# Kernel tuning notes

Measured on AMD Instinct MI355X. Metric: run time of the kernel, lower is better.

Reference implementation:

```python
import jax, jax.numpy as jnp
import numpy as np

A = 128       # atom_fea_len
NBR = 41      # nbr_fea_len
H = 128       # h_fea_len_dist == h_fea_len_const
NCONV = 3
EPS = 1e-5    # BatchNorm eps


def leaky(x):
    return jnp.where(x >= 0, x, 0.01 * x)  # LeakyReLU(0.01)


def bn(x2d, g, b):
    # training-mode BatchNorm1d: batch statistics over dim 0 (biased variance)
    mu = x2d.mean(0)
    var = x2d.var(0)
    return g * (x2d - mu) * jax.lax.rsqrt(var + EPS) + b


def setup_inputs() -> dict:
    N, M = 20000, 12
    key = jax.random.key(0)
    ks = jax.random.split(key, 24)
    s = 0.02
    in2 = 2 * A + NBR  # 297
    d = {}
    d["atom_fea"] = jax.random.normal(ks[0], (N, 92), jnp.float32)
    d["nbr_fea"] = jax.random.uniform(ks[1], (N, M, NBR), dtype=jnp.float32)
    d["nbr_fea_offset"] = jax.random.normal(ks[2], (N, M, 3), jnp.float32)
    d["atom_pos"] = jax.random.normal(ks[3], (N, 3), jnp.float32) * 3.0
    d["cells"] = jnp.eye(3, dtype=jnp.float32) * 10.0 + 0.1 * jax.random.normal(ks[4], (3, 3), jnp.float32)
    d["nbr_fea_idx"] = jax.random.randint(ks[5], (N, M), 0, N)
    # embedding
    d["emb_W"] = s * jax.random.normal(ks[6], (A, 92), jnp.float32)
    d["emb_b"] = jnp.zeros((A,), jnp.float32)
    # conv layers (stacked)
    d["convs_W"] = s * jax.random.normal(ks[7], (NCONV, 2 * A, in2), jnp.float32)
    d["convs_b"] = jnp.zeros((NCONV, 2 * A), jnp.float32)
    d["convs_bn1_g"] = jnp.ones((NCONV, 2 * A), jnp.float32)
    d["convs_bn1_b"] = jnp.zeros((NCONV, 2 * A), jnp.float32)
    d["convs_bn2_g"] = jnp.ones((NCONV, A), jnp.float32)
    d["convs_bn2_b"] = jnp.zeros((NCONV, A), jnp.float32)
    # bond_distance head
    d["dist_W"] = s * jax.random.normal(ks[8], (H, in2), jnp.float32)
    d["dist_b"] = jnp.zeros((H,), jnp.float32)
    d["dist_bn_g"] = jnp.ones((H,), jnp.float32)
    d["dist_bn_b"] = jnp.zeros((H,), jnp.float32)
    d["dist2_W"] = s * jax.random.normal(ks[9], (1, H), jnp.float32)
    d["dist2_b"] = jnp.zeros((1,), jnp.float32)
    # bond_constant head
    d["const_W"] = s * jax.random.normal(ks[10], (H, in2), jnp.float32)
    d["const_b"] = jnp.zeros((H,), jnp.float32)
    d["const_bn_g"] = jnp.ones((H,), jnp.float32)
    d["const_bn_b"] = jnp.zeros((H,), jnp.float32)
    d["const2_W"] = s * jax.random.normal(ks[11], (1, H), jnp.float32)
    d["const2_b"] = jnp.zeros((1,), jnp.float32)
    return d


def _forward(atom_fea, nbr_fea, nbr_fea_offset, atom_pos, cells,
             emb_W, emb_b, convs_W, convs_b, convs_bn1_g, convs_bn1_b,
             convs_bn2_g, convs_bn2_b, dist_W, dist_b, dist_bn_g, dist_bn_b,
             dist2_W, dist2_b, const_W, const_b, const_bn_g, const_bn_b,
             const2_W, const2_b, nbr_fea_idx):
    N, M = nbr_fea_idx.shape
    af = atom_fea @ emb_W.T + emb_b  # (N, A) embedding

    # get_distance: PBC distance using fractional offsets and the cell matrix
    nbr_abs = atom_pos[nbr_fea_idx] + jnp.einsum('nmk,kd->nmd', nbr_fea_offset, cells)
    dvec = nbr_abs - atom_pos[:, None, :]
    distance = jnp.sqrt(jnp.sum(dvec * dvec, -1, keepdims=True) + 1e-12)  # (N, M, 1)

    # conv layers: gather -> concat -> linear -> bn -> gate -> sum -> bn -> residual
    for i in range(NCONV):
        total = jnp.concatenate([
            jnp.broadcast_to(af[:, None, :], (N, M, A)),
            af[nbr_fea_idx],
            nbr_fea], axis=2)                                   # (N, M, 2A+NBR)
        g = jnp.einsum('nmf,of->nmo', total, convs_W[i]) + convs_b[i]  # (N, M, 2A)
        g = bn(g.reshape(-1, 2 * A), convs_bn1_g[i], convs_bn1_b[i]).reshape(N, M, 2 * A)
        nbr_filter = jax.nn.sigmoid(g[..., :A])
        nbr_core = leaky(g[..., A:])
        summed = bn((nbr_filter * nbr_core).sum(1), convs_bn2_g[i], convs_bn2_b[i])
        af = leaky(af + summed)

    # bond features
    bond_fea = jnp.concatenate([
        jnp.broadcast_to(af[:, None, :], (N, M, A)),
        af[nbr_fea_idx],
        nbr_fea], axis=2)  # (N, M, 2A+NBR)

    # bond_distance head (LeakyReLU activations)
    bd = jnp.einsum('nmf,hf->nmh', bond_fea, dist_W) + dist_b
    bd = leaky(bn(bd.reshape(-1, H), dist_bn_g, dist_bn_b).reshape(N, M, H))
    bd = leaky(jnp.einsum('nmh,oh->nmo', bd, dist2_W) + dist2_b + distance)  # (N, M, 1)

    # bond_constant head (Softplus activations)
    bc = jnp.einsum('nmf,hf->nmh', bond_fea, const_W) + const_b
    bc = jax.nn.softplus(bn(bc.reshape(-1, H), const_bn_g, const_bn_b).reshape(N, M, H))
    bc = jax.nn.softplus(jnp.einsum('nmh,oh->nmo', bc, const2_W) + const2_b)  # (N, M, 1)

    return jnp.concatenate([bd, bc], axis=-1)  # (N, M, 2)


def reference(atom_fea, nbr_fea, nbr_fea_offset, atom_pos, cells,
              emb_W, emb_b, convs_W, convs_b, convs_bn1_g, convs_bn1_b,
              convs_bn2_g, convs_bn2_b, dist_W, dist_b, dist_bn_g, dist_bn_b,
              dist2_W, dist2_b, const_W, const_b, const_bn_g, const_bn_b,
              const2_W, const2_b, nbr_fea_idx):
    return _forward(atom_fea, nbr_fea, nbr_fea_offset, atom_pos, cells,
                    emb_W, emb_b, convs_W, convs_b, convs_bn1_g, convs_bn1_b,
                    convs_bn2_g, convs_bn2_b, dist_W, dist_b, dist_bn_g, dist_bn_b,
                    dist2_W, dist2_b, const_W, const_b, const_bn_g, const_bn_b,
                    const2_W, const2_b, nbr_fea_idx)
```

## Files before the change

kernel.cpp:

```cpp
#include <hip/hip_runtime.h>
#include <hip/hip_bf16.h>
#include <math.h>

typedef __hip_bfloat16 bf16;

#define AFEA 128
#define NBRF 41
#define IN2 297
#define KP 320
#define TSTR 328
#define ROWS 64
#define P1 64
#define P2 16

typedef __attribute__((ext_vector_type(8))) short bf16x8;
typedef __attribute__((ext_vector_type(4))) float f32x4;

__device__ __forceinline__ unsigned short bfbits(float x) {
    bf16 h = __float2bfloat16(x);
    return *(unsigned short*)&h;
}
__device__ __forceinline__ unsigned int pack2(float x, float y) {
    return (unsigned int)bfbits(x) | ((unsigned int)bfbits(y) << 16);
}
__device__ __forceinline__ float blo(unsigned int u) { return __uint_as_float(u << 16); }
__device__ __forceinline__ float bhi(unsigned int u) { return __uint_as_float(u & 0xffff0000u); }
__device__ __forceinline__ float leakyf(float x) { return x >= 0.f ? x : 0.01f * x; }
__device__ __forceinline__ float sigmoid_fast(float x) { return 1.f / (1.f + __expf(-x)); }
__device__ __forceinline__ float softplus_fast(float x) {
    return fmaxf(x, 0.f) + __logf(1.f + __expf(-fabsf(x)));
}

__global__ void nbr16_kernel(const float* __restrict__ nbr, unsigned short* __restrict__ nbr16,
                             int NM)
{
    int i = blockIdx.x * blockDim.x + threadIdx.x;
    if (i >= NM * 64) return;
    int k = i & 63, e = i >> 6;
    nbr16[i] = (k < NBRF) ? bfbits(nbr[(size_t)e * NBRF + k]) : 0;
}

__global__ __launch_bounds__(256) void embed_kernel(
    const float* __restrict__ xf, const float* __restrict__ W,
    const float* __restrict__ b, float* __restrict__ af,
    unsigned short* __restrict__ af16, int N)
{
    __shared__ float W_s[92 * 128];
    __shared__ float xs[16 * 92];
    int t = threadIdx.x;
    int n0 = blockIdx.x * 16;
    for (int i = t; i < 92 * 128; i += 256) {
        int o = i / 92, k = i - o * 92;
        W_s[k * 128 + o] = W[i];
    }
    for (int i = t; i < 16 * 92; i += 256) {
        int a = i / 92, k = i - a * 92;
        int n = n0 + a;
        xs[i] = (n < N) ? xf[(size_t)n * 92 + k] : 0.f;
    }
    __syncthreads();
    int o = t & 127, h = t >> 7;
    float bias = b[o];
    for (int a = h; a < 16; a += 2) {
        int n = n0 + a;
        if (n >= N) break;
        float acc = bias;
        const float* xr = xs + a * 92;
        #pragma unroll 4
        for (int k = 0; k < 92; k++) acc += xr[k] * W_s[k * 128 + o];
        af[(size_t)n * AFEA + o] = acc;
        af16[(size_t)n * AFEA + o] = bfbits(acc);
    }
}

__global__ void prep_kernel(const float* __restrict__ Wa, size_t offA,
                            const float* __restrict__ Wsrc, size_t offB,
                            unsigned short* __restrict__ Wb,
                            float* __restrict__ zbuf, int nz)
{
    int i = blockIdx.x * blockDim.x + threadIdx.x;
    if (i < nz) zbuf[i] = 0.f;
    if (i >= KP * 256) return;
    int t32 = i & 31;
    int c = (i >> 5) & 255;
    int kc = i >> 13;
    int k = kc * 32 + t32;
    float v = 0.f;
    if (k < IN2) v = (c < 128) ? Wa[offA + (size_t)c * IN2 + k]
                               : Wsrc[offB + (size_t)(c - 128) * IN2 + k];
    Wb[i] = bfbits(v);
}

__global__ __launch_bounds__(256, 3) void gemm_mfma_kernel(
    const unsigned short* __restrict__ af16, const unsigned short* __restrict__ nbr16,
    const int* __restrict__ idx, const unsigned short* __restrict__ Wb,
    const float* __restrict__ bias_a, size_t boffA,
    const float* __restrict__ bias_b, size_t boffB,
    unsigned short* __restrict__ g_t, float* __restrict__ part1,
    int NM, int M)
{
    __shared__ unsigned short a_tile[ROWS * TSTR];
    const int t = threadIdx.x;
    const int e0 = blockIdx.x * ROWS;

    const int l = t & 63, w = t >> 6;
    const int m16 = l & 15, q = l >> 4;
    const int colbase = w * 64;
    const unsigned short* bbase = Wb + (size_t)(colbase + m16) * 32 + q * 8;

    {
        int row = t >> 2, p = t & 3;
        int e = e0 + row;
        int n = e / M;
        int j = idx[e];
        const uint4* srcn = (const uint4*)(af16 + (size_t)n * AFEA);
        const uint4* srcj = (const uint4*)(af16 + (size_t)j * AFEA);
        const uint4* srcb = (const uint4*)(nbr16 + (size_t)e * 64);
        uint4* dst = (uint4*)(a_tile + row * TSTR);
        #pragma unroll
        for (int u = 0; u < 4; u++) dst[p + 4 * u] = srcn[p + 4 * u];
        #pragma unroll
        for (int u = 0; u < 4; u++) dst[16 + p + 4 * u] = srcj[p + 4 * u];
        #pragma unroll
        for (int u = 0; u < 2; u++) dst[32 + p + 4 * u] = srcb[p + 4 * u];
    }

    bf16x8 bcur[4], bnxt[4];
    #pragma unroll
    for (int ct = 0; ct < 4; ct++)
        bcur[ct] = *(const bf16x8*)(bbase + ct * 512);
    #pragma unroll
    for (int ct = 0; ct < 4; ct++)
        bnxt[ct] = *(const bf16x8*)(bbase + 8192 + ct * 512);

    __syncthreads();

    f32x4 acc[4][4];
    #pragma unroll
    for (int rt = 0; rt < 4; rt++)
        #pragma unroll
        for (int ct = 0; ct < 4; ct++) acc[rt][ct] = (f32x4)0.f;

    const unsigned short* abase = a_tile + m16 * TSTR + q * 8;

    #pragma unroll
    for (int kc = 0; kc < KP / 32; kc++) {
        bf16x8 a[4], b2[4];
        if (kc < KP / 32 - 2) {
            #pragma unroll
            for (int ct = 0; ct < 4; ct++)
                b2[ct] = *(const bf16x8*)(bbase + (kc + 2) * 8192 + ct * 512);
        }
        #pragma unroll
        for (int rt = 0; rt < 4; rt++)
            a[rt] = *(const bf16x8*)(abase + rt * 16 * TSTR + kc * 32);
        #pragma unroll
        for (int rt = 0; rt < 4; rt++)
            #pragma unroll
            for (int ct = 0; ct < 4; ct++)
                acc[rt][ct] = __builtin_amdgcn_mfma_f32_16x16x32_bf16(
                    a[rt], bcur[ct], acc[rt][ct], 0, 0, 0);
        if (kc < KP / 32 - 1) {
            #pragma unroll
            for (int ct = 0; ct < 4; ct++) bcur[ct] = bnxt[ct];
        }
        if (kc < KP / 32 - 2) {
            #pragma unroll
            for (int ct = 0; ct < 4; ct++) bnxt[ct] = b2[ct];
        }
    }

    float* pp = part1 + (size_t)(blockIdx.x & (P1 - 1)) * 512;
    #pragma unroll
    for (int ct = 0; ct < 4; ct++) {
        int col = colbase + ct * 16 + m16;
        float bias = (col < 128) ? bias_a[boffA + col] : bias_b[boffB + col - 128];
        float ps = 0.f, pq = 0.f;
        #pragma unroll
        for (int rt = 0; rt < 4; rt++) {
            float v0 = acc[rt][ct][0] + bias;
            float v1 = acc[rt][ct][1] + bias;
            float v2 = acc[rt][ct][2] + bias;
            float v3 = acc[rt][ct][3] + bias;
            ps += (v0 + v1) + (v2 + v3);
            pq += (v0 * v0 + v1 * v1) + (v2 * v2 + v3 * v3);
            uint2 pk;
            pk.x = pack2(v0, v1);
            pk.y = pack2(v2, v3);
            *(uint2*)(g_t + (size_t)col * NM + e0 + rt * 16 + q * 4) = pk;
        }
        ps += __shfl_xor(ps, 16); ps += __shfl_xor(ps, 32);
        pq += __shfl_xor(pq, 16); pq += __shfl_xor(pq, 32);
        if (q == 0) {
            atomicAdd(&pp[col], ps);
            atomicAdd(&pp[256 + col], pq);
        }
    }
}

__global__ __launch_bounds__(256) void gate_kernel(
    const unsigned short* __restrict__ gt, const float* __restrict__ part1,
    const float* __restrict__ gamma, const float* __restrict__ beta,
    float* __restrict__ summed, float* __restrict__ part2,
    float cnt1, int N, int M, int NM)
{
    __shared__ float affA[4 * 16], affC[4 * 16];
    int t = threadIdx.x, w = t >> 6, l = t & 63;
    int cp0 = (blockIdx.x & 3) * 16 + w * 4;
    int fch0 = 2 * cp0;

    if (l < 16) {
        int ch = (l < 8) ? (fch0 + l) : (128 + fch0 + (l - 8));
        float s = 0.f, qq = 0.f;
        #pragma unroll 8
        for (int p = 0; p < P1; p++) {
            s += part1[(size_t)p * 512 + ch];
            qq += part1[(size_t)p * 512 + 256 + ch];
        }
        float mean = s / cnt1;
        float var = fmaxf(qq / cnt1 - mean * mean, 0.f);
        float a = gamma[ch] * rsqrtf(var + 1e-5f);
        affA[w * 16 + l] = a;
        affC[w * 16 + l] = beta[ch] - mean * a;
    }
    __syncthreads();

    int n = (blockIdx.x >> 2) * 64 + l;
    bool act = (n < N);
    size_t col0 = (size_t)n * M;
    float* pp = part2 + (size_t)(blockIdx.x & (P2 - 1)) * 256;
    #pragma unroll
    for (int cpi = 0; cpi < 4; cpi++) {
        int chf = fch0 + 2 * cpi;
        int chc = 128 + chf;
        float s0 = 0.f, s1 = 0.f;
        if (act) {
            const uint2* rf0 = (const uint2*)(gt + (size_t)chf * NM + col0);
            const uint2* rf1 = (const uint2*)(gt + (size_t)(chf + 1) * NM + col0);
            const uint2* rc0 = (const uint2*)(gt + (size_t)chc * NM + col0);
            const uint2* rc1 = (const uint2*)(gt + (size_t)(chc + 1) * NM + col0);
            float aF0 = affA[w * 16 + 2 * cpi],     cF0 = affC[w * 16 + 2 * cpi];
            float aF1 = affA[w * 16 + 2 * cpi + 1], cF1 = affC[w * 16 + 2 * cpi + 1];
            float aC0 = affA[w * 16 + 8 + 2 * cpi],     cC0 = affC[w * 16 + 8 + 2 * cpi];
            float aC1 = affA[w * 16 + 8 + 2 * cpi + 1], cC1 = affC[w * 16 + 8 + 2 * cpi + 1];
            #pragma unroll
            for (int u = 0; u < 3; u++) {
                uint2 f0 = rf0[u], f1 = rf1[u], k0 = rc0[u], k1 = rc1[u];
                #pragma unroll
                for (int h = 0; h < 4; h++) {
                    unsigned int fw0 = (h < 2) ? f0.x : f0.y;
                    unsigned int fw1 = (h < 2) ? f1.x : f1.y;
                    unsigned int kw0 = (h < 2) ? k0.x : k0.y;
                    unsigned int kw1 = (h < 2) ? k1.x : k1.y;
                    float gf0 = (h & 1) ? bhi(fw0) : blo(fw0);
                    float gf1 = (h & 1) ? bhi(fw1) : blo(fw1);
                    float gc0 = (h & 1) ? bhi(kw0) : blo(kw0);
                    float gc1 = (h & 1) ? bhi(kw1) : blo(kw1);
                    s0 += sigmoid_fast(fmaf(aF0, gf0, cF0)) * leakyf(fmaf(aC0, gc0, cC0));
                    s1 += sigmoid_fast(fmaf(aF1, gf1, cF1)) * leakyf(fmaf(aC1, gc1, cC1));
                }
            }
            *(float2*)(summed + (size_t)n * AFEA + chf) = make_float2(s0, s1);
        }
        float q0 = s0 * s0, q1 = s1 * s1;
        #pragma unroll
        for (int sft = 32; sft > 0; sft >>= 1) {
            s0 += __shfl_xor(s0, sft);
            s1 += __shfl_xor(s1, sft);
            q0 += __shfl_xor(q0, sft);
            q1 += __shfl_xor(q1, sft);
        }
        if (l == 0) {
            atomicAdd(&pp[chf], s0);
            atomicAdd(&pp[chf + 1], s1);
            atomicAdd(&pp[128 + chf], q0);
            atomicAdd(&pp[128 + chf + 1], q1);
        }
    }
}

__global__ __launch_bounds__(256) void afup_kernel(
    float* __restrict__ af, unsigned short* __restrict__ af16,
    const float* __restrict__ summed, const float* __restrict__ part2,
    const float* __restrict__ gamma2, const float* __restrict__ beta2,
    float cnt2, int total)
{
    __shared__ float a2s[128], c2s[128];
    int t = threadIdx.x;
    if (t < 128) {
        float s = 0.f, qq = 0.f;
        #pragma unroll
        for (int p = 0; p < P2; p++) {
            s += part2[(size_t)p * 256 + t];
            qq += part2[(size_t)p * 256 + 128 + t];
        }
        float mean = s / cnt2;
        float var = fmaxf(qq / cnt2 - mean * mean, 0.f);
        float a = gamma2[t] * rsqrtf(var + 1e-5f);
        a2s[t] = a;
        c2s[t] = beta2[t] - mean * a;
    }
    __syncthreads();
    int o = t & 127;
    float a2 = a2s[o], c2 = c2s[o];
    int base = blockIdx.x * 2048 + t;
    #pragma unroll
    for (int k = 0; k < 8; k++) {
        int i = base + k * 256;
        if (i < total) {
            float v = af[i] + a2 * summed[i] + c2;
            v = (v >= 0.f) ? v : 0.01f * v;
            af[i] = v;
            af16[i] = bfbits(v);
        }
    }
}

__global__ __launch_bounds__(256) void head_kernel(
    const unsigned short* __restrict__ gt, const float* __restrict__ part1,
    const float* __restrict__ dbg, const float* __restrict__ cbg,
    const float* __restrict__ dbb, const float* __restrict__ cbb,
    const float* __restrict__ w2d, const float* __restrict__ b2d,
    const float* __restrict__ w2c, const float* __restrict__ b2c,
    const float* __restrict__ pos, const float* __restrict__ off,
    const float* __restrict__ cells, const int* __restrict__ idx,
    float* __restrict__ out, float cnt1, int NM, int M)
{
    __shared__ float a_s[256], c_s[256], w_s[256];
    int t = threadIdx.x;
    {
        float s = 0.f, qq = 0.f;
        #pragma unroll 8
        for (int p = 0; p < P1; p++) {
            s += part1[(size_t)p * 512 + t];
            qq += part1[(size_t)p * 512 + 256 + t];
        }
        float mean = s / cnt1;
        float var = fmaxf(qq / cnt1 - mean * mean, 0.f);
        float g  = (t < 128) ? dbg[t] : cbg[t - 128];
        float be = (t < 128) ? dbb[t] : cbb[t - 128];
        float a = g * rsqrtf(var + 1e-5f);
        a_s[t] = a;
        c_s[t] = be - mean * a;
        w_s[t] = (t < 128) ? w2d[t] : w2c[t - 128];
    }
    __syncthreads();

    int e = blockIdx.x * 512 + t * 2;
    if (e >= NM) return;
    float sd0 = 0.f, sd1 = 0.f, sc0 = 0.f, sc1 = 0.f;
    #pragma unroll 4
    for (int ch = 0; ch < 128; ch++) {
        unsigned int u = *(const unsigned int*)(gt + (size_t)ch * NM + e);
        float a = a_s[ch], c = c_s[ch], wv = w_s[ch];
        sd0 += leakyf(fmaf(a, blo(u), c)) * wv;
        sd1 += leakyf(fmaf(a, bhi(u), c)) * wv;
    }
    #pragma unroll 4
    for (int ch = 128; ch < 256; ch++) {
        unsigned int u = *(const unsigned int*)(gt + (size_t)ch * NM + e);
        float a = a_s[ch], c = c_s[ch], wv = w_s[ch];
        sc0 += softplus_fast(fmaf(a, blo(u), c)) * wv;
        sc1 += softplus_fast(fmaf(a, bhi(u), c)) * wv;
    }
    float dist[2];
    #pragma unroll
    for (int h = 0; h < 2; h++) {
        int eb = e + h;
        int n = eb / M;
        int j = idx[eb];
        float o0 = off[(size_t)eb * 3 + 0];
        float o1 = off[(size_t)eb * 3 + 1];
        float o2 = off[(size_t)eb * 3 + 2];
        float d0 = o0 * cells[0] + o1 * cells[3] + o2 * cells[6] + pos[(size_t)j * 3 + 0] - pos[(size_t)n * 3 + 0];
        float d1 = o0 * cells[1] + o1 * cells[4] + o2 * cells[7] + pos[(size_t)j * 3 + 1] - pos[(size_t)n * 3 + 1];
        float d2 = o0 * cells[2] + o1 * cells[5] + o2 * cells[8] + pos[(size_t)j * 3 + 2] - pos[(size_t)n * 3 + 2];
        dist[h] = sqrtf(d0 * d0 + d1 * d1 + d2 * d2 + 1e-12f);
    }
    float bd = b2d[0], bc = b2c[0];
    float4 o4;
    o4.x = leakyf(sd0 + bd + dist[0]);
    o4.y = softplus_fast(sc0 + bc);
    o4.z = leakyf(sd1 + bd + dist[1]);
    o4.w = softplus_fast(sc1 + bc);
    *(float4*)(out + (size_t)e * 2) = o4;
}

extern "C" void kernel_launch(void* const* d_in, const int* in_sizes, int n_in,
                              void* d_out, int out_size, void* d_ws, size_t ws_size,
                              hipStream_t stream) {
    const float* atom_fea   = (const float*)d_in[0];
    const float* nbr_fea    = (const float*)d_in[1];
    const float* nbr_off    = (const float*)d_in[2];
    const float* atom_pos   = (const float*)d_in[3];
    const float* cells      = (const float*)d_in[4];
    const int*   idx        = (const int*)d_in[5];
    const float* emb_W      = (const float*)d_in[6];
    const float* emb_b      = (const float*)d_in[7];
    const float* convs_W    = (const float*)d_in[8];
    const float* convs_b    = (const float*)d_in[9];
    const float* bn1g       = (const float*)d_in[10];
    const float* bn1b       = (const float*)d_in[11];
    const float* bn2g       = (const float*)d_in[12];
    const float* bn2b       = (const float*)d_in[13];
    const float* dist_W     = (const float*)d_in[14];
    const float* dist_b     = (const float*)d_in[15];
    const float* dist_bn_g  = (const float*)d_in[16];
    const float* dist_bn_b  = (const float*)d_in[17];
    const float* dist2_W    = (const float*)d_in[18];
    const float* dist2_b    = (const float*)d_in[19];
    const float* const_W    = (const float*)d_in[20];
    const float* const_b    = (const float*)d_in[21];
    const float* const_bn_g = (const float*)d_in[22];
    const float* const_bn_b = (const float*)d_in[23];
    const float* const2_W   = (const float*)d_in[24];
    const float* const2_b   = (const float*)d_in[25];

    const int N  = in_sizes[0] / 92;
    const int M  = in_sizes[5] / N;
    const int NM = N * M;

    char* ws = (char*)d_ws;
    size_t off = 0;
    float* af             = (float*)(ws + off); off += (size_t)N * AFEA * 4;
    float* summed         = (float*)(ws + off); off += (size_t)N * AFEA * 4;
    unsigned short* af16  = (unsigned short*)(ws + off); off += (size_t)N * AFEA * 2;
    unsigned short* Wb    = (unsigned short*)(ws + off); off += (size_t)256 * KP * 2;
    float* part1          = (float*)(ws + off); off += (size_t)P1 * 512 * 4;
    float* part2          = (float*)(ws + off); off += (size_t)P2 * 256 * 4;
    unsigned short* g_t   = (unsigned short*)(ws + off); off += (size_t)NM * 256 * 2;
    unsigned short* nbr16 = (unsigned short*)(ws + off); off += (size_t)NM * 64 * 2;

    const int NPART = P1 * 512 + P2 * 256;

    nbr16_kernel<<<(NM * 64 + 255) / 256, 256, 0, stream>>>(nbr_fea, nbr16, NM);
    embed_kernel<<<(N + 15) / 16, 256, 0, stream>>>(atom_fea, emb_W, emb_b, af, af16, N);

    const int gblocks = NM / ROWS;
    const int gateblocks = ((N + 63) / 64) * 4;
    const int prepblocks = (256 * KP + 255) / 256;

    for (int i = 0; i < 3; i++) {
        size_t wo  = (size_t)i * 256 * IN2;
        size_t bo  = (size_t)i * 256;
        size_t b2o = (size_t)i * 128;

        prep_kernel<<<prepblocks, 256, 0, stream>>>(
            convs_W, wo, convs_W, wo + (size_t)128 * IN2, Wb, part1, NPART);
        gemm_mfma_kernel<<<gblocks, 256, 0, stream>>>(
            af16, nbr16, idx, Wb, convs_b, bo, convs_b, bo + 128,
            g_t, part1, NM, M);
        gate_kernel<<<gateblocks, 256, 0, stream>>>(
            g_t, part1, bn1g + bo, bn1b + bo, summed, part2, (float)NM, N, M, NM);
        afup_kernel<<<(N * AFEA + 2047) / 2048, 256, 0, stream>>>(
            af, af16, summed, part2, bn2g + b2o, bn2b + b2o, (float)N, N * AFEA);
    }

    {
        prep_kernel<<<prepblocks, 256, 0, stream>>>(
            dist_W, 0, const_W, 0, Wb, part1, P1 * 512);
        gemm_mfma_kernel<<<gblocks, 256, 0, stream>>>(
            af16, nbr16, idx, Wb, dist_b, 0, const_b, 0,
            g_t, part1, NM, M);
        head_kernel<<<(NM + 511) / 512, 256, 0, stream>>>(
            g_t, part1, dist_bn_g, const_bn_g, dist_bn_b, const_bn_b,
            dist2_W, dist2_b, const2_W, const2_b,
            atom_pos, nbr_off, cells, idx, (float*)d_out, (float)NM, NM, M);
    }
}
```

Baseline: 683.4 us.

## Load GEMM A operands directly from global memory, dropping the LDS tile

The gathered A rows (atom self, neighbor atom, bond features) are no longer staged through a shared-memory tile. Each lane now loads its MFMA fragments straight from global memory using precomputed per-row offsets. The manual double-buffered prefetch of weight fragments is also removed, and the launch-bounds occupancy hint is raised from 3 to 4 blocks. The goal is to avoid LDS traffic and the block barrier and to let more blocks run per CU. In exchange the global loads are less coalesced, each wave reloads rows the other waves also read, and load latency now sits directly in front of the MFMAs without explicit prefetching.

New measurement: 861.3 us. +26.0%, slower.

```diff
diff --git a/kernel.cpp b/kernel.cpp
--- a/kernel.cpp
+++ b/kernel.cpp
@@ -8,7 +8,6 @@
 #define NBRF 41
 #define IN2 297
 #define KP 320
-#define TSTR 328
 #define ROWS 64
 #define P1 64
 #define P2 16
@@ -91,7 +90,7 @@
     Wb[i] = bfbits(v);
 }
 
-__global__ __launch_bounds__(256, 3) void gemm_mfma_kernel(
+__global__ __launch_bounds__(256, 4) void gemm_mfma_kernel(
     const unsigned short* __restrict__ af16, const unsigned short* __restrict__ nbr16,
     const int* __restrict__ idx, const unsigned short* __restrict__ Wb,
     const float* __restrict__ bias_a, size_t boffA,
@@ -99,41 +98,23 @@
     unsigned short* __restrict__ g_t, float* __restrict__ part1,
     int NM, int M)
 {
-    __shared__ unsigned short a_tile[ROWS * TSTR];
     const int t = threadIdx.x;
-    const int e0 = blockIdx.x * ROWS;
-
     const int l = t & 63, w = t >> 6;
     const int m16 = l & 15, q = l >> 4;
+    const int e0 = blockIdx.x * ROWS;
     const int colbase = w * 64;
     const unsigned short* bbase = Wb + (size_t)(colbase + m16) * 32 + q * 8;
 
-    {
-        int row = t >> 2, p = t & 3;
-        int e = e0 + row;
+    int offn[4], offj[4], offb[4];
+    #pragma unroll
+    for (int rt = 0; rt < 4; rt++) {
+        int e = e0 + rt * 16 + m16;
         int n = e / M;
         int j = idx[e];
-        const uint4* srcn = (const uint4*)(af16 + (size_t)n * AFEA);
-        const uint4* srcj = (const uint4*)(af16 + (size_t)j * AFEA);
-        const uint4* srcb = (const uint4*)(nbr16 + (size_t)e * 64);
-        uint4* dst = (uint4*)(a_tile + row * TSTR);
-        #pragma unroll
-        for (int u = 0; u < 4; u++) dst[p + 4 * u] = srcn[p + 4 * u];
-        #pragma unroll
-        for (int u = 0; u < 4; u++) dst[16 + p + 4 * u] = srcj[p + 4 * u];
-        #pragma unroll
-        for (int u = 0; u < 2; u++) dst[32 + p + 4 * u] = srcb[p + 4 * u];
-    }
-
-    bf16x8 bcur[4], bnxt[4];
-    #pragma unroll
-    for (int ct = 0; ct < 4; ct++)
-        bcur[ct] = *(const bf16x8*)(bbase + ct * 512);
-    #pragma unroll
-    for (int ct = 0; ct < 4; ct++)
-        bnxt[ct] = *(const bf16x8*)(bbase + 8192 + ct * 512);
-
-    __syncthreads();
+        offn[rt] = n * AFEA + q * 8;
+        offj[rt] = j * AFEA + q * 8;
+        offb[rt] = e * 64 + q * 8;
+    }
 
     f32x4 acc[4][4];
     #pragma unroll
@@ -141,33 +122,24 @@
         #pragma unroll
         for (int ct = 0; ct < 4; ct++) acc[rt][ct] = (f32x4)0.f;
 
-    const unsigned short* abase = a_tile + m16 * TSTR + q * 8;
-
     #pragma unroll
     for (int kc = 0; kc < KP / 32; kc++) {
-        bf16x8 a[4], b2[4];
-        if (kc < KP / 32 - 2) {
-            #pragma unroll
-            for (int ct = 0; ct < 4; ct++)
-                b2[ct] = *(const bf16x8*)(bbase + (kc + 2) * 8192 + ct * 512);
-        }
-        #pragma unroll
-        for (int rt = 0; rt < 4; rt++)
-            a[rt] = *(const bf16x8*)(abase + rt * 16 * TSTR + kc * 32);
+        bf16x8 a[4], b[4];
+        #pragma unroll
+        for (int ct = 0; ct < 4; ct++)
+            b[ct] = *(const bf16x8*)(bbase + (size_t)kc * 8192 + ct * 512);
+        #pragma unroll
+        for (int rt = 0; rt < 4; rt++) {
+            if (kc < 4)       a[rt] = *(const bf16x8*)(af16 + offn[rt] + kc * 32);
+            else if (kc < 8)  a[rt] = *(const bf16x8*)(af16 + offj[rt] + (kc - 4) * 32);
+            else              a[rt] = *(const bf16x8*)(nbr16 + offb[rt] + (kc - 8) * 32);
+        }
         #pragma unroll
         for (int rt = 0; rt < 4; rt++)
             #pragma unroll
             for (int ct = 0; ct < 4; ct++)
                 acc[rt][ct] = __builtin_amdgcn_mfma_f32_16x16x32_bf16(
-                    a[rt], bcur[ct], acc[rt][ct], 0, 0, 0);
-        if (kc < KP / 32 - 1) {
-            #pragma unroll
-            for (int ct = 0; ct < 4; ct++) bcur[ct] = bnxt[ct];
-        }
-        if (kc < KP / 32 - 2) {
-            #pragma unroll
-            for (int ct = 0; ct < 4; ct++) bnxt[ct] = b2[ct];
-        }
+                    a[rt], b[ct], acc[rt][ct], 0, 0, 0);
     }
 
     float* pp = part1 + (size_t)(blockIdx.x & (P1 - 1)) * 512;
```

## Drop fp32 atom features, read neighbor features directly, shrink GEMM LDS tile

Applied to the files above, without the earlier changes.

Removes the fp32 copy of atom features and keeps only bf16, so the residual update reads the previous value from bf16. The GEMM no longer stages neighbor-bond features through shared memory: the last two K-chunks load their A operand straight from global memory. The LDS tile shrinks accordingly, B prefetch depth drops from two to one, and the occupancy hint rises to 4. This trims LDS and registers and cuts memory traffic, but it rounds the residual stream to bf16 between layers and exposes global-load latency in the final K chunks.

Measured after the change: 756.8 us. 10.7% more time.

```diff
diff --git a/kernel.cpp b/kernel.cpp
--- a/kernel.cpp
+++ b/kernel.cpp
@@ -8,8 +8,7 @@
 #define NBRF 41
 #define IN2 297
 #define KP 320
-#define TSTR 328
-#define ROWS 64
+#define ASTR 264
 #define P1 64
 #define P2 16
 
@@ -19,6 +18,9 @@
 __device__ __forceinline__ unsigned short bfbits(float x) {
     bf16 h = __float2bfloat16(x);
     return *(unsigned short*)&h;
+}
+__device__ __forceinline__ float us2f(unsigned short u) {
+    return __uint_as_float((unsigned int)u << 16);
 }
 __device__ __forceinline__ unsigned int pack2(float x, float y) {
     return (unsigned int)bfbits(x) | ((unsigned int)bfbits(y) << 16);
@@ -42,8 +44,7 @@
 
 __global__ __launch_bounds__(256) void embed_kernel(
     const float* __restrict__ xf, const float* __restrict__ W,
-    const float* __restrict__ b, float* __restrict__ af,
-    unsigned short* __restrict__ af16, int N)
+    const float* __restrict__ b, unsigned short* __restrict__ af16, int N)
 {
     __shared__ float W_s[92 * 128];
     __shared__ float xs[16 * 92];
@@ -68,13 +69,12 @@
         const float* xr = xs + a * 92;
         #pragma unroll 4
         for (int k = 0; k < 92; k++) acc += xr[k] * W_s[k * 128 + o];
-        af[(size_t)n * AFEA + o] = acc;
         af16[(size_t)n * AFEA + o] = bfbits(acc);
     }
 }
 
 __global__ void prep_kernel(const float* __restrict__ Wa, size_t offA,
-                            const float* __restrict__ Wsrc, size_t offB,
+                            const float* __restrict__ Wb2, size_t offB,
                             unsigned short* __restrict__ Wb,
                             float* __restrict__ zbuf, int nz)
 {
@@ -87,11 +87,11 @@
     int k = kc * 32 + t32;
     float v = 0.f;
     if (k < IN2) v = (c < 128) ? Wa[offA + (size_t)c * IN2 + k]
-                               : Wsrc[offB + (size_t)(c - 128) * IN2 + k];
+                               : Wb2[offB + (size_t)(c - 128) * IN2 + k];
     Wb[i] = bfbits(v);
 }
 
-__global__ __launch_bounds__(256, 3) void gemm_mfma_kernel(
+__global__ __launch_bounds__(256, 4) void gemm_mfma_kernel(
     const unsigned short* __restrict__ af16, const unsigned short* __restrict__ nbr16,
     const int* __restrict__ idx, const unsigned short* __restrict__ Wb,
     const float* __restrict__ bias_a, size_t boffA,
@@ -99,10 +99,9 @@
     unsigned short* __restrict__ g_t, float* __restrict__ part1,
     int NM, int M)
 {
-    __shared__ unsigned short a_tile[ROWS * TSTR];
+    __shared__ unsigned short a_tile[64 * ASTR];
     const int t = threadIdx.x;
-    const int e0 = blockIdx.x * ROWS;
-
+    const int e0 = blockIdx.x * 64;
     const int l = t & 63, w = t >> 6;
     const int m16 = l & 15, q = l >> 4;
     const int colbase = w * 64;
@@ -115,23 +114,17 @@
         int j = idx[e];
         const uint4* srcn = (const uint4*)(af16 + (size_t)n * AFEA);
         const uint4* srcj = (const uint4*)(af16 + (size_t)j * AFEA);
-        const uint4* srcb = (const uint4*)(nbr16 + (size_t)e * 64);
-        uint4* dst = (uint4*)(a_tile + row * TSTR);
+        uint4* dst = (uint4*)(a_tile + row * ASTR);
         #pragma unroll
         for (int u = 0; u < 4; u++) dst[p + 4 * u] = srcn[p + 4 * u];
         #pragma unroll
         for (int u = 0; u < 4; u++) dst[16 + p + 4 * u] = srcj[p + 4 * u];
-        #pragma unroll
-        for (int u = 0; u < 2; u++) dst[32 + p + 4 * u] = srcb[p + 4 * u];
-    }
-
-    bf16x8 bcur[4], bnxt[4];
+    }
+
+    bf16x8 bcur[4];
     #pragma unroll
     for (int ct = 0; ct < 4; ct++)
         bcur[ct] = *(const bf16x8*)(bbase + ct * 512);
-    #pragma unroll
-    for (int ct = 0; ct < 4; ct++)
-        bnxt[ct] = *(const bf16x8*)(bbase + 8192 + ct * 512);
 
     __syncthreads();
 
@@ -141,19 +134,26 @@
         #pragma unroll
         for (int ct = 0; ct < 4; ct++) acc[rt][ct] = (f32x4)0.f;
 
-    const unsigned short* abase = a_tile + m16 * TSTR + q * 8;
+    const unsigned short* abase = a_tile + m16 * ASTR + q * 8;
 
     #pragma unroll
     for (int kc = 0; kc < KP / 32; kc++) {
-        bf16x8 a[4], b2[4];
-        if (kc < KP / 32 - 2) {
+        bf16x8 a[4], bn[4];
+        if (kc < KP / 32 - 1) {
             #pragma unroll
             for (int ct = 0; ct < 4; ct++)
-                b2[ct] = *(const bf16x8*)(bbase + (kc + 2) * 8192 + ct * 512);
-        }
-        #pragma unroll
-        for (int rt = 0; rt < 4; rt++)
-            a[rt] = *(const bf16x8*)(abase + rt * 16 * TSTR + kc * 32);
+                bn[ct] = *(const bf16x8*)(bbase + (kc + 1) * 8192 + ct * 512);
+        }
+        if (kc < 8) {
+            #pragma unroll
+            for (int rt = 0; rt < 4; rt++)
+                a[rt] = *(const bf16x8*)(abase + rt * 16 * ASTR + kc * 32);
+        } else {
+            #pragma unroll
+            for (int rt = 0; rt < 4; rt++)
+                a[rt] = *(const bf16x8*)(nbr16 + (size_t)(e0 + rt * 16 + m16) * 64
+                                         + (kc - 8) * 32 + q * 8);
+        }
         #pragma unroll
         for (int rt = 0; rt < 4; rt++)
             #pragma unroll
@@ -162,11 +162,7 @@
                     a[rt], bcur[ct], acc[rt][ct], 0, 0, 0);
         if (kc < KP / 32 - 1) {
             #pragma unroll
-            for (int ct = 0; ct < 4; ct++) bcur[ct] = bnxt[ct];
-        }
-        if (kc < KP / 32 - 2) {
-            #pragma unroll
-            for (int ct = 0; ct < 4; ct++) bnxt[ct] = b2[ct];
+            for (int ct = 0; ct < 4; ct++) bcur[ct] = bn[ct];
         }
     }
 
@@ -280,8 +276,8 @@
 }
 
 __global__ __launch_bounds__(256) void afup_kernel(
-    float* __restrict__ af, unsigned short* __restrict__ af16,
-    const float* __restrict__ summed, const float* __restrict__ part2,
+    unsigned short* __restrict__ af16, const float* __restrict__ summed,
+    const float* __restrict__ part2,
     const float* __restrict__ gamma2, const float* __restrict__ beta2,
     float cnt2, int total)
 {
@@ -308,9 +304,8 @@
     for (int k = 0; k < 8; k++) {
         int i = base + k * 256;
         if (i < total) {
-            float v = af[i] + a2 * summed[i] + c2;
+            float v = us2f(af16[i]) + a2 * summed[i] + c2;
             v = (v >= 0.f) ? v : 0.01f * v;
-            af[i] = v;
             af16[i] = bfbits(v);
         }
     }
@@ -422,9 +417,8 @@
 
     char* ws = (char*)d_ws;
     size_t off = 0;
-    float* af             = (float*)(ws + off); off += (size_t)N * AFEA * 4;
+    unsigned short* af16  = (unsigned short*)(ws + off); off += (size_t)N * AFEA * 2;
     float* summed         = (float*)(ws + off); off += (size_t)N * AFEA * 4;
-    unsigned short* af16  = (unsigned short*)(ws + off); off += (size_t)N * AFEA * 2;
     unsigned short* Wb    = (unsigned short*)(ws + off); off += (size_t)256 * KP * 2;
     float* part1          = (float*)(ws + off); off += (size_t)P1 * 512 * 4;
     float* part2          = (float*)(ws + off); off += (size_t)P2 * 256 * 4;
@@ -434,9 +428,9 @@
     const int NPART = P1 * 512 + P2 * 256;
 
     nbr16_kernel<<<(NM * 64 + 255) / 256, 256, 0, stream>>>(nbr_fea, nbr16, NM);
-    embed_kernel<<<(N + 15) / 16, 256, 0, stream>>>(atom_fea, emb_W, emb_b, af, af16, N);
-
-    const int gblocks = NM / ROWS;
+    embed_kernel<<<(N + 15) / 16, 256, 0, stream>>>(atom_fea, emb_W, emb_b, af16, N);
+
+    const int gblocks = NM / 64;
     const int gateblocks = ((N + 63) / 64) * 4;
     const int prepblocks = (256 * KP + 255) / 256;
 
@@ -453,7 +447,7 @@
         gate_kernel<<<gateblocks, 256, 0, stream>>>(
             g_t, part1, bn1g + bo, bn1b + bo, summed, part2, (float)NM, N, M, NM);
         afup_kernel<<<(N * AFEA + 2047) / 2048, 256, 0, stream>>>(
-            af, af16, summed, part2, bn2g + b2o, bn2b + b2o, (float)N, N * AFEA);
+            af16, summed, part2, bn2g + b2o, bn2b + b2o, (float)N, N * AFEA);
     }
 
     {
```
